# Kernel optimization log

Hardware: AMD Instinct MI355X
Metric: run time of the kernel (lower is better)

Reference implementation:

```python
import jax, jax.numpy as jnp
import numpy as np

B, S, DIM, HEADS, MLP = 2, 2048, 1024, 16, 4096
DH = DIM // HEADS
LN_EPS = 1e-5


def layernorm(x, g, b):
    m = x.mean(-1, keepdims=True)
    v = ((x - m) ** 2).mean(-1, keepdims=True)
    return (x - m) / jnp.sqrt(v + LN_EPS) * g + b


def rope(x):
    # x: [B, H, S, dh]; interleaved-pair RoPE (rotary_embedding_torch convention)
    dh = x.shape[-1]
    s = x.shape[-2]
    inv_freq = 1.0 / (10000.0 ** (jnp.arange(0, dh, 2, dtype=jnp.float32) / dh))
    freqs = jnp.arange(s, dtype=jnp.float32)[:, None] * inv_freq[None, :]  # [S, dh/2]
    cos = jnp.repeat(jnp.cos(freqs), 2, axis=-1)  # [S, dh]
    sin = jnp.repeat(jnp.sin(freqs), 2, axis=-1)
    xp = x.reshape(x.shape[:-1] + (dh // 2, 2))
    x_rot = jnp.stack([-xp[..., 1], xp[..., 0]], axis=-1).reshape(x.shape)
    return x * cos + x_rot * sin


def setup_inputs() -> dict:
    key = jax.random.key(0)
    ks = jax.random.split(key, 10)
    w = 0.02
    return {
        "x": jax.random.normal(ks[0], (B, S, DIM), jnp.float32),
        "bias": jax.random.normal(ks[1], (B, S, S), jnp.float32) * 0.1,
        "ln1_g": jnp.ones((DIM,), jnp.float32),
        "ln1_b": jnp.zeros((DIM,), jnp.float32),
        "W_qkv": jax.random.normal(ks[2], (DIM, 3 * DIM), jnp.float32) * w,
        "W_o": jax.random.normal(ks[3], (DIM, DIM), jnp.float32) * w,
        "ln2_g": jnp.ones((DIM,), jnp.float32),
        "ln2_b": jnp.zeros((DIM,), jnp.float32),
        "W1": jax.random.normal(ks[4], (DIM, MLP), jnp.float32) * w,
        "b1": jnp.zeros((MLP,), jnp.float32),
        "W2": jax.random.normal(ks[5], (MLP, DIM), jnp.float32) * w,
        "b2": jnp.zeros((DIM,), jnp.float32),
        "pad_mask": jnp.zeros((B, S), jnp.int32),
    }


def reference(x, bias, ln1_g, ln1_b, W_qkv, W_o, ln2_g, ln2_b, W1, b1, W2, b2, pad_mask):
    b, s, d = x.shape
    h, dh = HEADS, DH
    res = x
    x1 = layernorm(x, ln1_g, ln1_b)
    qkv = (x1 @ W_qkv).reshape(b, s, h, 3 * dh)
    q, k, v = jnp.split(qkv, 3, axis=-1)            # each [B,S,H,dh]
    q = rope(q.transpose(0, 2, 1, 3))               # [B,H,S,dh]
    k = rope(k.transpose(0, 2, 1, 3))
    v = v.transpose(0, 2, 1, 3)
    scores = jnp.einsum("bhqd,bhkd->bhqk", q, k) * (dh ** -0.5)
    scores = scores + bias[:, None]                 # additive bias per batch
    key_mask = pad_mask.astype(bool)[:, None, None, :]
    scores = jnp.where(key_mask, -jnp.inf, scores)
    attn = jax.nn.softmax(scores, axis=-1)          # dropout = identity (eval)
    out = jnp.einsum("bhqk,bhkd->bhqd", attn, v)
    out = out.transpose(0, 2, 1, 3).reshape(b, s, d)
    x = res + out @ W_o
    res2 = x
    x2 = layernorm(x, ln2_g, ln2_b)
    mlp = jax.nn.gelu(x2 @ W1 + b1, approximate=False) @ W2 + b2
    return res2 + mlp
```

## Files before the change

kernel.cpp:

```cpp
#include <hip/hip_runtime.h>
#include <hip/hip_bf16.h>

#define B_   2
#define S_   2048
#define DIM_ 1024
#define H_   16
#define DH_  64
#define MLP_ 4096

typedef __bf16 bf16x8 __attribute__((ext_vector_type(8)));
typedef float  f32x4  __attribute__((ext_vector_type(4)));

__device__ __forceinline__ ushort f2bf(float f) {
    union { float f; unsigned u; } x; x.f = f;
    unsigned r = x.u + 0x7FFFu + ((x.u >> 16) & 1u);
    return (ushort)(r >> 16);
}
__device__ __forceinline__ float bf2f(ushort b) {
    union { unsigned u; float f; } x; x.u = ((unsigned)b) << 16;
    return x.f;
}

#define GLOAD_LDS16(gptr, lptr)                                                        \
    __builtin_amdgcn_global_load_lds(                                                  \
        (const __attribute__((address_space(1))) unsigned int*)(const void*)(gptr),    \
        (__attribute__((address_space(3))) unsigned int*)(void*)(lptr), 16, 0, 0)

#define MFMA_BF16(a, b, c) __builtin_amdgcn_mfma_f32_16x16x32_bf16((a), (b), (c), 0, 0, 0)

__global__ __launch_bounds__(256) void transpose_all(const float* __restrict__ Wqkv, ushort* __restrict__ Wqkvt,
                                                     const float* __restrict__ Wo,   ushort* __restrict__ Wot,
                                                     const float* __restrict__ W1,   ushort* __restrict__ W1t,
                                                     const float* __restrict__ W2,   ushort* __restrict__ W2t) {
    int id = blockIdx.x;
    const float* in; ushort* outp; int K, N, nx;
    if (id < 3072)      { in = Wqkv; outp = Wqkvt; K = 1024; N = 3072; nx = 96;  }
    else if (id < 4096) { id -= 3072; in = Wo; outp = Wot;  K = 1024; N = 1024; nx = 32;  }
    else if (id < 8192) { id -= 4096; in = W1; outp = W1t;  K = 1024; N = 4096; nx = 128; }
    else                { id -= 8192; in = W2; outp = W2t;  K = 4096; N = 1024; nx = 32;  }
    int n0 = (id % nx) * 32, k0 = (id / nx) * 32;
    __shared__ float t[32][33];
    int tx = threadIdx.x, ty = threadIdx.y;
#pragma unroll
    for (int r = 0; r < 32; r += 8)
        t[ty + r][tx] = in[(size_t)(k0 + ty + r) * N + n0 + tx];
    __syncthreads();
#pragma unroll
    for (int r = 0; r < 32; r += 8)
        outp[(size_t)(n0 + ty + r) * K + k0 + tx] = f2bf(t[tx][ty + r]);
}

__global__ __launch_bounds__(256) void vt_prep(const ushort* __restrict__ qkv,
                                               ushort* __restrict__ VT) {
    __shared__ ushort t[32][34];
    int s0 = blockIdx.x * 32, d0 = blockIdx.y * 32, bh = blockIdx.z;
    int h = bh & 15, b = bh >> 4;
    const ushort* src = qkv + (size_t)b * S_ * (3 * DIM_) + h * 192 + 128;
    int tx = threadIdx.x, ty = threadIdx.y;
#pragma unroll
    for (int r = 0; r < 32; r += 8)
        t[ty + r][tx] = src[(size_t)(s0 + ty + r) * (3 * DIM_) + d0 + tx];
    __syncthreads();
    ushort* dst = VT + ((size_t)bh * DH_ + d0) * S_ + s0;
#pragma unroll
    for (int r = 0; r < 32; r += 8)
        dst[(size_t)(ty + r) * S_ + tx] = t[tx][ty + r];
}

__global__ __launch_bounds__(256) void ln_kernel(const float* __restrict__ in,
                                                 const float* __restrict__ g,
                                                 const float* __restrict__ beta,
                                                 ushort* __restrict__ out) {
    int row = blockIdx.x;
    float4 v = reinterpret_cast<const float4*>(in + (size_t)row * DIM_)[threadIdx.x];
    float s = v.x + v.y + v.z + v.w;
    float s2 = v.x * v.x + v.y * v.y + v.z * v.z + v.w * v.w;
#pragma unroll
    for (int m = 1; m < 64; m <<= 1) { s += __shfl_xor(s, m); s2 += __shfl_xor(s2, m); }
    __shared__ float red[8];
    int wid = threadIdx.x >> 6;
    if ((threadIdx.x & 63) == 0) { red[wid] = s; red[4 + wid] = s2; }
    __syncthreads();
    s  = red[0] + red[1] + red[2] + red[3];
    s2 = red[4] + red[5] + red[6] + red[7];
    float mean = s * (1.f / DIM_);
    float var  = s2 * (1.f / DIM_) - mean * mean;
    float inv  = rsqrtf(var + 1e-5f);
    float4 gg = reinterpret_cast<const float4*>(g)[threadIdx.x];
    float4 bb = reinterpret_cast<const float4*>(beta)[threadIdx.x];
    ushort4 o;
    o.x = f2bf((v.x - mean) * inv * gg.x + bb.x);
    o.y = f2bf((v.y - mean) * inv * gg.y + bb.y);
    o.z = f2bf((v.z - mean) * inv * gg.z + bb.z);
    o.w = f2bf((v.w - mean) * inv * gg.w + bb.w);
    reinterpret_cast<ushort4*>(out + (size_t)row * DIM_)[threadIdx.x] = o;
}

template <int RM, int RN, bool BIAS, bool GELU, bool RES, bool OBF16>
__global__ __launch_bounds__(256) void gemm_bt(const ushort* __restrict__ A,
                                               const ushort* __restrict__ Bt,
                                               void* __restrict__ Cout,
                                               const float* __restrict__ bias,
                                               const float* __restrict__ resid,
                                               int M, int N, int K) {
    constexpr int BM = RM * 64, BN = RN * 64;
    __shared__ __align__(16) ushort As[2][BM * 32];
    __shared__ __align__(16) ushort Bs[2][BN * 32];
    int tid = threadIdx.x;
    int wid = tid >> 6, lane = tid & 63;
    int lr = lane & 15, lg = lane >> 4;

    int nbx = gridDim.x;
    int nwg = nbx * gridDim.y;
    int bid = blockIdx.y * nbx + blockIdx.x;
    int swz = (bid & 7) * (nwg >> 3) + (bid >> 3);
    int row0 = (swz / nbx) * BM, col0 = (swz % nbx) * BN;

    int wm = (wid >> 1) * (RM * 32), wn = (wid & 1) * (RN * 32);
    int srow = tid >> 2, scol = (tid & 3) * 8;

    f32x4 acc[RM * 2][RN * 2] = {};

    const ushort* gA = A + (size_t)(row0 + srow) * K + scol;
    const ushort* gB = Bt + (size_t)(col0 + srow) * K + scol;

    auto stage = [&](int buf, int kt) {
#pragma unroll
        for (int r = 0; r < RM; r++)
            GLOAD_LDS16(gA + (size_t)r * 64 * K + kt, As[buf] + r * 2048 + wid * 512);
#pragma unroll
        for (int r = 0; r < RN; r++)
            GLOAD_LDS16(gB + (size_t)r * 64 * K + kt, Bs[buf] + r * 2048 + wid * 512);
    };

    int nk = K >> 5;
    stage(0, 0);
    __syncthreads();

    for (int t = 0; t < nk; t++) {
        int cur = t & 1;
        if (t + 1 < nk) stage(cur ^ 1, (t + 1) << 5);
        bf16x8 af[RM * 2], bfr[RN * 2];
#pragma unroll
        for (int m = 0; m < RM * 2; m++)
            af[m] = *reinterpret_cast<const bf16x8*>(As[cur] + (wm + m * 16 + lr) * 32 + lg * 8);
#pragma unroll
        for (int n = 0; n < RN * 2; n++)
            bfr[n] = *reinterpret_cast<const bf16x8*>(Bs[cur] + (wn + n * 16 + lr) * 32 + lg * 8);
#pragma unroll
        for (int m = 0; m < RM * 2; m++)
#pragma unroll
            for (int n = 0; n < RN * 2; n++)
                acc[m][n] = MFMA_BF16(af[m], bfr[n], acc[m][n]);
        __syncthreads();
    }

#pragma unroll
    for (int m = 0; m < RM * 2; m++) {
#pragma unroll
        for (int n = 0; n < RN * 2; n++) {
            int col = col0 + wn + n * 16 + lr;
#pragma unroll
            for (int i = 0; i < 4; i++) {
                int row = row0 + wm + m * 16 + lg * 4 + i;
                float v = acc[m][n][i];
                if (BIAS) v += bias[col];
                if (GELU) v = 0.5f * v * (1.f + erff(v * 0.70710678118f));
                if (RES)  v += resid[(size_t)row * N + col];
                if (OBF16) ((ushort*)Cout)[(size_t)row * N + col] = f2bf(v);
                else       ((float*)Cout)[(size_t)row * N + col] = v;
            }
        }
    }
}

__global__ __launch_bounds__(256) void rope_table(float2* __restrict__ tab) {
    int i = blockIdx.x * 256 + threadIdx.x;
    int s = i >> 5, p = i & 31;
    float invf = __expf(-((float)(2 * p) / 64.f) * logf(10000.f));
    float a = (float)s * invf;
    tab[i] = make_float2(cosf(a), sinf(a));
}

__global__ __launch_bounds__(256) void rope_apply(const ushort* __restrict__ qkv,
                                                  const float2* __restrict__ tab,
                                                  ushort* __restrict__ Qo,
                                                  ushort* __restrict__ Ko) {
    int i = blockIdx.x * 256 + threadIdx.x;
    int p = i & 31;
    int s = (i >> 5) & (S_ - 1);
    int h = (i >> 16) & (H_ - 1);
    int b = i >> 20;
    float2 cs = tab[(s << 5) + p];
    size_t src = ((size_t)(b * S_ + s)) * (3 * DIM_) + h * 192 + 2 * p;
    size_t dst = (((size_t)(b * H_ + h) * S_) + s) * DH_ + 2 * p;
    float q0 = bf2f(qkv[src]), q1 = bf2f(qkv[src + 1]);
    Qo[dst]     = f2bf(q0 * cs.x - q1 * cs.y);
    Qo[dst + 1] = f2bf(q1 * cs.x + q0 * cs.y);
    float k0 = bf2f(qkv[src + 64]), k1 = bf2f(qkv[src + 65]);
    Ko[dst]     = f2bf(k0 * cs.x - k1 * cs.y);
    Ko[dst + 1] = f2bf(k1 * cs.x + k0 * cs.y);
}

__global__ __launch_bounds__(256) void attn_kernel(const ushort* __restrict__ Q,
                                                   const ushort* __restrict__ Kr,
                                                   const ushort* __restrict__ VT,
                                                   const float* __restrict__ bias,
                                                   const int* __restrict__ pad,
                                                   ushort* __restrict__ Out) {
    int bx = blockIdx.x;
    int qt = bx & 31, h = (bx >> 5) & 15, b = bx >> 9;
    __shared__ __align__(16) ushort Ks[64 * 72];
    __shared__ __align__(16) ushort Vs[64 * 72];
    __shared__ __align__(16) ushort Ps[64 * 72];
    int tid = threadIdx.x, wid = tid >> 6, lane = tid & 63;
    int lr = lane & 15, lg = lane >> 4;
    int q0 = qt * 64;
    const ushort* Qb = Q + ((size_t)(b * H_ + h) * S_) * DH_;
    const ushort* Kb = Kr + ((size_t)(b * H_ + h) * S_) * DH_;
    const ushort* Vb = VT + ((size_t)(b * H_ + h) * DH_) * S_;
    const float*  bb = bias + (size_t)b * S_ * S_;
    const int*    pb = pad + b * S_;

    bf16x8 qf[2];
#pragma unroll
    for (int ks = 0; ks < 2; ks++)
        qf[ks] = *reinterpret_cast<const bf16x8*>(
            Qb + (size_t)(q0 + wid * 16 + lr) * DH_ + ks * 32 + lg * 8);

    float mrow[4], lrow[4];
#pragma unroll
    for (int i = 0; i < 4; i++) { mrow[i] = -3e38f; lrow[i] = 0.f; }
    f32x4 o[4] = {};

    int sr = tid >> 3, sc = (tid & 7) * 8;
    const float scale = 0.125f;

    for (int kv0 = 0; kv0 < S_; kv0 += 64) {
        __syncthreads();
#pragma unroll
        for (int cc = 0; cc < 2; cc++) {
            int r = cc * 32 + sr;
            *reinterpret_cast<bf16x8*>(Ks + r * 72 + sc) =
                *reinterpret_cast<const bf16x8*>(Kb + (size_t)(kv0 + r) * DH_ + sc);
            *reinterpret_cast<bf16x8*>(Vs + r * 72 + sc) =
                *reinterpret_cast<const bf16x8*>(Vb + (size_t)r * S_ + kv0 + sc);
        }
        __syncthreads();

        f32x4 sa[4] = {};
#pragma unroll
        for (int n = 0; n < 4; n++) {
            bf16x8 k0 = *reinterpret_cast<const bf16x8*>(Ks + (n * 16 + lr) * 72 + lg * 8);
            bf16x8 k1 = *reinterpret_cast<const bf16x8*>(Ks + (n * 16 + lr) * 72 + 32 + lg * 8);
            sa[n] = MFMA_BF16(qf[0], k0, sa[n]);
            sa[n] = MFMA_BF16(qf[1], k1, sa[n]);
        }

        int pm[4];
#pragma unroll
        for (int n = 0; n < 4; n++) pm[n] = pb[kv0 + n * 16 + lr];

#pragma unroll
        for (int i = 0; i < 4; i++) {
            const float* brow = bb + (size_t)(q0 + wid * 16 + lg * 4 + i) * S_ + kv0;
            float sv[4];
            float rmax = -3e38f;
#pragma unroll
            for (int n = 0; n < 4; n++) {
                float s = sa[n][i] * scale + brow[n * 16 + lr];
                if (pm[n]) s = -1e30f;
                sv[n] = s;
                rmax = fmaxf(rmax, s);
            }
#pragma unroll
            for (int msk = 1; msk < 16; msk <<= 1) rmax = fmaxf(rmax, __shfl_xor(rmax, msk));
            float mnew = fmaxf(mrow[i], rmax);
            float resc = __expf(mrow[i] - mnew);
            mrow[i] = mnew;
            float ls = 0.f;
            int prow = (i << 2) | lg;
#pragma unroll
            for (int n = 0; n < 4; n++) {
                float p = __expf(sv[n] - mnew);
                ls += p;
                Ps[(wid * 16 + prow) * 72 + n * 16 + lr] = f2bf(p);
            }
            lrow[i] = lrow[i] * resc + ls;
#pragma unroll
            for (int fn = 0; fn < 4; fn++) o[fn][i] *= resc;
        }

        int plr = ((lr & 3) << 2) | (lr >> 2);
        bf16x8 pf0 = *reinterpret_cast<const bf16x8*>(Ps + (wid * 16 + plr) * 72 + lg * 8);
        bf16x8 pf1 = *reinterpret_cast<const bf16x8*>(Ps + (wid * 16 + plr) * 72 + 32 + lg * 8);

#pragma unroll
        for (int fn = 0; fn < 4; fn++) {
            bf16x8 v0 = *reinterpret_cast<const bf16x8*>(Vs + (fn * 16 + lr) * 72 + lg * 8);
            bf16x8 v1 = *reinterpret_cast<const bf16x8*>(Vs + (fn * 16 + lr) * 72 + 32 + lg * 8);
            o[fn] = MFMA_BF16(pf0, v0, o[fn]);
            o[fn] = MFMA_BF16(pf1, v1, o[fn]);
        }
    }

#pragma unroll
    for (int i = 0; i < 4; i++)
#pragma unroll
        for (int msk = 1; msk < 16; msk <<= 1) lrow[i] += __shfl_xor(lrow[i], msk);

#pragma unroll
    for (int fn = 0; fn < 4; fn++)
#pragma unroll
        for (int i = 0; i < 4; i++) {
            int qrow = q0 + wid * 16 + lg * 4 + i;
            Out[(size_t)(b * S_ + qrow) * DIM_ + h * DH_ + fn * 16 + lr] =
                f2bf(o[fn][i] / lrow[i]);
        }
}

extern "C" void kernel_launch(void* const* d_in, const int* in_sizes, int n_in,
                              void* d_out, int out_size, void* d_ws, size_t ws_size,
                              hipStream_t stream) {
    const float* x    = (const float*)d_in[0];
    const float* bias = (const float*)d_in[1];
    const float* ln1g = (const float*)d_in[2];
    const float* ln1b = (const float*)d_in[3];
    const float* Wqkv = (const float*)d_in[4];
    const float* Wo   = (const float*)d_in[5];
    const float* ln2g = (const float*)d_in[6];
    const float* ln2b = (const float*)d_in[7];
    const float* W1   = (const float*)d_in[8];
    const float* b1   = (const float*)d_in[9];
    const float* W2   = (const float*)d_in[10];
    const float* b2   = (const float*)d_in[11];
    const int*   pad  = (const int*)d_in[12];
    float* out = (float*)d_out;

    char* ws = (char*)d_ws;
    size_t off = 0;
    auto alloc = [&](size_t bytes) {
        char* p = ws + off;
        off += (bytes + 255) & ~(size_t)255;
        return (void*)p;
    };
    ushort* x1    = (ushort*)alloc((size_t)4096 * 1024 * 2);
    ushort* Wqkvt = (ushort*)alloc((size_t)3072 * 1024 * 2);
    ushort* qkv   = (ushort*)alloc((size_t)4096 * 3072 * 2);
    float2* tab   = (float2*)alloc((size_t)S_ * 32 * 8);
    ushort* Qr    = (ushort*)alloc((size_t)B_ * H_ * S_ * DH_ * 2);
    ushort* Kr2   = (ushort*)alloc((size_t)B_ * H_ * S_ * DH_ * 2);
    ushort* attnO = (ushort*)alloc((size_t)4096 * 1024 * 2);
    ushort* Wot   = (ushort*)alloc((size_t)1024 * 1024 * 2);
    float*  xmid  = (float*)alloc((size_t)4096 * 1024 * 4);
    ushort* x2    = (ushort*)alloc((size_t)4096 * 1024 * 2);
    ushort* W1t   = (ushort*)alloc((size_t)4096 * 1024 * 2);
    ushort* h1    = (ushort*)alloc((size_t)4096 * 4096 * 2);
    ushort* W2t   = (ushort*)alloc((size_t)1024 * 4096 * 2);
    ushort* VT    = h1;

    dim3 tb(32, 8);
    transpose_all<<<12288, tb, 0, stream>>>(Wqkv, Wqkvt, Wo, Wot, W1, W1t, W2, W2t);

    ln_kernel<<<4096, 256, 0, stream>>>(x, ln1g, ln1b, x1);

    gemm_bt<2, 2, false, false, false, true><<<dim3(24, 32), 256, 0, stream>>>(
        x1, Wqkvt, qkv, nullptr, nullptr, 4096, 3072, 1024);

    rope_table<<<(S_ * 32) / 256, 256, 0, stream>>>(tab);
    rope_apply<<<(B_ * H_ * S_ * 32) / 256, 256, 0, stream>>>(qkv, tab, Qr, Kr2);
    vt_prep<<<dim3(S_ / 32, DH_ / 32, B_ * H_), tb, 0, stream>>>(qkv, VT);

    attn_kernel<<<B_ * H_ * (S_ / 64), 256, 0, stream>>>(Qr, Kr2, VT, bias, pad, attnO);

    gemm_bt<1, 2, false, false, true, false><<<dim3(8, 64), 256, 0, stream>>>(
        attnO, Wot, xmid, nullptr, x, 4096, 1024, 1024);

    ln_kernel<<<4096, 256, 0, stream>>>(xmid, ln2g, ln2b, x2);

    gemm_bt<2, 2, true, true, false, true><<<dim3(32, 32), 256, 0, stream>>>(
        x2, W1t, h1, b1, nullptr, 4096, 4096, 1024);

    gemm_bt<1, 2, true, false, true, false><<<dim3(8, 64), 256, 0, stream>>>(
        h1, W2t, out, b2, xmid, 4096, 1024, 4096);
}
```

Before: 333.7 us.

## Fuse RoPE and V transpose into the QKV GEMM epilogue

```diff
diff --git a/kernel.cpp b/kernel.cpp
--- a/kernel.cpp
+++ b/kernel.cpp
@@ -48,23 +48,6 @@
 #pragma unroll
     for (int r = 0; r < 32; r += 8)
         outp[(size_t)(n0 + ty + r) * K + k0 + tx] = f2bf(t[tx][ty + r]);
-}
-
-__global__ __launch_bounds__(256) void vt_prep(const ushort* __restrict__ qkv,
-                                               ushort* __restrict__ VT) {
-    __shared__ ushort t[32][34];
-    int s0 = blockIdx.x * 32, d0 = blockIdx.y * 32, bh = blockIdx.z;
-    int h = bh & 15, b = bh >> 4;
-    const ushort* src = qkv + (size_t)b * S_ * (3 * DIM_) + h * 192 + 128;
-    int tx = threadIdx.x, ty = threadIdx.y;
-#pragma unroll
-    for (int r = 0; r < 32; r += 8)
-        t[ty + r][tx] = src[(size_t)(s0 + ty + r) * (3 * DIM_) + d0 + tx];
-    __syncthreads();
-    ushort* dst = VT + ((size_t)bh * DH_ + d0) * S_ + s0;
-#pragma unroll
-    for (int r = 0; r < 32; r += 8)
-        dst[(size_t)(ty + r) * S_ + tx] = t[tx][ty + r];
 }
 
 __global__ __launch_bounds__(256) void ln_kernel(const float* __restrict__ in,
@@ -174,32 +157,106 @@
     }
 }
 
+__global__ __launch_bounds__(256) void gemm_qkv(const ushort* __restrict__ A,
+                                                const ushort* __restrict__ Bt,
+                                                const float2* __restrict__ tab,
+                                                ushort* __restrict__ Qr,
+                                                ushort* __restrict__ Kr,
+                                                ushort* __restrict__ VT) {
+    const int K = DIM_, N = 3 * DIM_;
+    __shared__ __align__(16) ushort As[2][128 * 32];
+    __shared__ __align__(16) ushort Bs[2][128 * 32];
+    int tid = threadIdx.x;
+    int wid = tid >> 6, lane = tid & 63;
+    int lr = lane & 15, lg = lane >> 4;
+
+    int nbx = gridDim.x;
+    int nwg = nbx * gridDim.y;
+    int bid = blockIdx.y * nbx + blockIdx.x;
+    int swz = (bid & 7) * (nwg >> 3) + (bid >> 3);
+    int row0 = (swz / nbx) * 128, col0 = (swz % nbx) * 128;
+
+    int wm = (wid >> 1) * 64, wn = (wid & 1) * 64;
+    int srow = tid >> 2, scol = (tid & 3) * 8;
+
+    f32x4 acc[4][4] = {};
+
+    const ushort* gA = A + (size_t)(row0 + srow) * K + scol;
+    const ushort* gB = Bt + (size_t)(col0 + srow) * K + scol;
+
+    auto stage = [&](int buf, int kt) {
+#pragma unroll
+        for (int r = 0; r < 2; r++)
+            GLOAD_LDS16(gA + (size_t)r * 64 * K + kt, As[buf] + r * 2048 + wid * 512);
+#pragma unroll
+        for (int r = 0; r < 2; r++)
+            GLOAD_LDS16(gB + (size_t)r * 64 * K + kt, Bs[buf] + r * 2048 + wid * 512);
+    };
+
+    int nk = K >> 5;
+    stage(0, 0);
+    __syncthreads();
+
+    for (int t = 0; t < nk; t++) {
+        int cur = t & 1;
+        if (t + 1 < nk) stage(cur ^ 1, (t + 1) << 5);
+        bf16x8 af[4], bfr[4];
+#pragma unroll
+        for (int m = 0; m < 4; m++)
+            af[m] = *reinterpret_cast<const bf16x8*>(As[cur] + (wm + m * 16 + lr) * 32 + lg * 8);
+#pragma unroll
+        for (int n = 0; n < 4; n++)
+            bfr[n] = *reinterpret_cast<const bf16x8*>(Bs[cur] + (wn + n * 16 + lr) * 32 + lg * 8);
+#pragma unroll
+        for (int m = 0; m < 4; m++)
+#pragma unroll
+            for (int n = 0; n < 4; n++)
+                acc[m][n] = MFMA_BF16(af[m], bfr[n], acc[m][n]);
+        __syncthreads();
+    }
+
+#pragma unroll
+    for (int n = 0; n < 4; n++) {
+        int colb = col0 + wn + n * 16;
+        int h    = colb / 192;
+        int off  = colb % 192;
+        int typ  = off >> 6;
+        int d    = (off & 63) + lr;
+#pragma unroll
+        for (int m = 0; m < 4; m++) {
+            if (typ < 2) {
+                ushort* qk = (typ == 0) ? Qr : Kr;
+#pragma unroll
+                for (int i = 0; i < 4; i++) {
+                    int row = row0 + wm + m * 16 + lg * 4 + i;
+                    int b = row >> 11, s = row & (S_ - 1);
+                    float v  = acc[m][n][i];
+                    float pv = __shfl_xor(v, 1);
+                    float2 cs = tab[(s << 5) + (d >> 1)];
+                    float r = v * cs.x + ((d & 1) ? pv : -pv) * cs.y;
+                    qk[((size_t)(b * H_ + h) * S_ + s) * DH_ + d] = f2bf(r);
+                }
+            } else {
+                int row = row0 + wm + m * 16 + lg * 4;
+                int b = row >> 11, s = row & (S_ - 1);
+                ushort4 o4;
+                o4.x = f2bf(acc[m][n][0]);
+                o4.y = f2bf(acc[m][n][1]);
+                o4.z = f2bf(acc[m][n][2]);
+                o4.w = f2bf(acc[m][n][3]);
+                *reinterpret_cast<ushort4*>(
+                    VT + ((size_t)(b * H_ + h) * DH_ + d) * S_ + s) = o4;
+            }
+        }
+    }
+}
+
 __global__ __launch_bounds__(256) void rope_table(float2* __restrict__ tab) {
     int i = blockIdx.x * 256 + threadIdx.x;
     int s = i >> 5, p = i & 31;
     float invf = __expf(-((float)(2 * p) / 64.f) * logf(10000.f));
     float a = (float)s * invf;
     tab[i] = make_float2(cosf(a), sinf(a));
-}
-
-__global__ __launch_bounds__(256) void rope_apply(const ushort* __restrict__ qkv,
-                                                  const float2* __restrict__ tab,
-                                                  ushort* __restrict__ Qo,
-                                                  ushort* __restrict__ Ko) {
-    int i = blockIdx.x * 256 + threadIdx.x;
-    int p = i & 31;
-    int s = (i >> 5) & (S_ - 1);
-    int h = (i >> 16) & (H_ - 1);
-    int b = i >> 20;
-    float2 cs = tab[(s << 5) + p];
-    size_t src = ((size_t)(b * S_ + s)) * (3 * DIM_) + h * 192 + 2 * p;
-    size_t dst = (((size_t)(b * H_ + h) * S_) + s) * DH_ + 2 * p;
-    float q0 = bf2f(qkv[src]), q1 = bf2f(qkv[src + 1]);
-    Qo[dst]     = f2bf(q0 * cs.x - q1 * cs.y);
-    Qo[dst + 1] = f2bf(q1 * cs.x + q0 * cs.y);
-    float k0 = bf2f(qkv[src + 64]), k1 = bf2f(qkv[src + 65]);
-    Ko[dst]     = f2bf(k0 * cs.x - k1 * cs.y);
-    Ko[dst + 1] = f2bf(k1 * cs.x + k0 * cs.y);
 }
 
 __global__ __launch_bounds__(256) void attn_kernel(const ushort* __restrict__ Q,
@@ -346,7 +403,6 @@
     };
     ushort* x1    = (ushort*)alloc((size_t)4096 * 1024 * 2);
     ushort* Wqkvt = (ushort*)alloc((size_t)3072 * 1024 * 2);
-    ushort* qkv   = (ushort*)alloc((size_t)4096 * 3072 * 2);
     float2* tab   = (float2*)alloc((size_t)S_ * 32 * 8);
     ushort* Qr    = (ushort*)alloc((size_t)B_ * H_ * S_ * DH_ * 2);
     ushort* Kr2   = (ushort*)alloc((size_t)B_ * H_ * S_ * DH_ * 2);
@@ -362,14 +418,11 @@
     dim3 tb(32, 8);
     transpose_all<<<12288, tb, 0, stream>>>(Wqkv, Wqkvt, Wo, Wot, W1, W1t, W2, W2t);
 
+    rope_table<<<(S_ * 32) / 256, 256, 0, stream>>>(tab);
+
     ln_kernel<<<4096, 256, 0, stream>>>(x, ln1g, ln1b, x1);
 
-    gemm_bt<2, 2, false, false, false, true><<<dim3(24, 32), 256, 0, stream>>>(
-        x1, Wqkvt, qkv, nullptr, nullptr, 4096, 3072, 1024);
-
-    rope_table<<<(S_ * 32) / 256, 256, 0, stream>>>(tab);
-    rope_apply<<<(B_ * H_ * S_ * 32) / 256, 256, 0, stream>>>(qkv, tab, Qr, Kr2);
-    vt_prep<<<dim3(S_ / 32, DH_ / 32, B_ * H_), tb, 0, stream>>>(qkv, VT);
+    gemm_qkv<<<dim3(24, 32), 256, 0, stream>>>(x1, Wqkvt, tab, Qr, Kr2, VT);
 
     attn_kernel<<<B_ * H_ * (S_ / 64), 256, 0, stream>>>(Qr, Kr2, VT, bias, pad, attnO);
 
```

Result: no change. 332.5 us, median of 2 (-0.4%).
